# Performance work log

Hardware: AMD Instinct MI355X
Metric: run time of the kernel (lower is better)

## Reference

```python
import jax, jax.numpy as jnp
import numpy as np

DIM = 20
N = 200000
E = 6400000
ITERATIONS = 3


def setup_inputs() -> dict:
    key = jax.random.key(0)
    ks = jax.random.split(key, 20)
    inp = {
        "h": jax.random.normal(ks[0], (N, DIM), dtype=jnp.float32),
        "node2depth": jax.random.randint(ks[1], (N,), 0, 5, dtype=jnp.int32),
        "edge_src": jax.random.randint(ks[2], (E,), 0, N, dtype=jnp.int32),
        "edge_dst": jax.random.randint(ks[3], (E,), 0, N, dtype=jnp.int32),
    }
    # Six DIM x DIM Linear layers (weight stored [out,in] like torch, plus bias)
    scale = 1.0 / np.sqrt(DIM)
    names = ["Wz", "Uz", "Wr", "Ur", "Wh", "Uh"]
    for j, nm in enumerate(names):
        inp[nm + "_w"] = jax.random.uniform(ks[4 + 2 * j], (DIM, DIM), jnp.float32, -scale, scale)
        inp[nm + "_b"] = jax.random.uniform(ks[5 + 2 * j], (DIM,), jnp.float32, -scale, scale)
    return inp


def _linear(x, w, b):
    return x @ w.T + b


def reference(h, Wz_w, Wz_b, Uz_w, Uz_b, Wr_w, Wr_b, Ur_w, Ur_b,
              Wh_w, Wh_b, Uh_w, Uh_b, node2depth, edge_src, edge_dst):
    active = None
    for i in range(ITERATIONS):
        # active set shrinks as i grows (depth + i <= ITERATIONS)
        active = (node2depth + i) <= ITERATIONS  # [N] bool
        af = active.astype(h.dtype)
        # x[u] = sum over neighbors v of h[v], counting only active src AND active dst
        msg = h[edge_src] * af[edge_src][:, None]          # [E, DIM]
        x = jax.ops.segment_sum(msg, edge_dst, num_segments=N)  # [N, DIM]
        x = x * af[:, None]
        z = jax.nn.sigmoid(_linear(x, Wz_w, Wz_b) + _linear(h, Uz_w, Uz_b))
        r = jax.nn.sigmoid(_linear(x, Wr_w, Wr_b) + _linear(h, Ur_w, Ur_b))
        h_cand = jnp.tanh(_linear(x, Wh_w, Wh_b) + _linear(r * h, Uh_w, Uh_b))
        h_new = z * h + (1.0 - z) * h_cand
        # inactive nodes are dropped from the dict in the original; since the
        # active set only shrinks, keeping their old h is equivalent
        h = jnp.where(active[:, None], h_new, h)
    # original returns only nodes active at the last iteration; zero out the rest
    return jnp.where(active[:, None], h, jnp.zeros_like(h))
```

## Files before the change

### kernel.cpp

```cpp
#include <hip/hip_runtime.h>

#define DIM    20
#define NN     200000
#define EE     6400000
#define ITERS  3
#define BLOCK  256

#define NODES_PER_FINE   64
#define NFINE            3125
#define NCOARSE          98
#define FINE_PER_COARSE  32

#define TILE1            2048
#define IPT1             8

#define TILE             4096
#define IPT              16

#define CAP1             67584
#define NT2P             17
#define CAP2             2304
#define PIPT             9

#define XSTRIDE          21

typedef unsigned int u32;

__device__ __forceinline__ u32 pack_bf16x2(float a, float b) {
    u32 ua = __float_as_uint(a);
    u32 ub = __float_as_uint(b);
    ua = (ua + 0x7FFFu + ((ua >> 16) & 1u)) >> 16;
    ub = (ub + 0x7FFFu + ((ub >> 16) & 1u)) & 0xFFFF0000u;
    return ua | ub;
}

__global__ __launch_bounds__(BLOCK) void setup(const float* __restrict__ h,
                                               const int* __restrict__ depth,
                                               u32* __restrict__ hbA,
                                               u32* __restrict__ hbC,
                                               u32* __restrict__ CT,
                                               int* __restrict__ coarse_cursor,
                                               int* __restrict__ fine_cursor,
                                               int* __restrict__ gcur) {
    int g = blockIdx.x * BLOCK + threadIdx.x;
    if (g < NCOARSE) coarse_cursor[g] = g * CAP1;
    if (g < NFINE)   fine_cursor[g]   = g * CAP2;
    if (g == 0) *gcur = 0;
    if (g < NN / 8) {
        int4 a = *(const int4*)(depth + g * 8);
        int4 b = *(const int4*)(depth + g * 8 + 4);
        CT[g] = ((u32)a.x & 7u)        | (((u32)a.y & 7u) << 4)
              | (((u32)a.z & 7u) << 8) | (((u32)a.w & 7u) << 12)
              | (((u32)b.x & 7u) << 16)| (((u32)b.y & 7u) << 20)
              | (((u32)b.z & 7u) << 24)| (((u32)b.w & 7u) << 28);
    }
    int node = g >> 3, s = g & 7;
    if (depth[node] > ITERS) return;
    float2 f = *(const float2*)(h + (size_t)node * DIM + s * 2);
    hbA[(size_t)node * 8 + s] = pack_bf16x2(f.x, f.y);
    if (s < 2) {
        float2 fc = *(const float2*)(h + (size_t)node * DIM + 16 + s * 2);
        hbC[(size_t)node * 2 + s] = pack_bf16x2(fc.x, fc.y);
    }
}

__global__ __launch_bounds__(BLOCK) void p1_split(const int* __restrict__ esrc,
                                                  const int* __restrict__ edst,
                                                  int* __restrict__ coarse_cursor,
                                                  u32* __restrict__ buf1) {
    __shared__ u32 hist[NCOARSE];
    __shared__ u32 lbase[NCOARSE];
    __shared__ u32 gbase[NCOARSE];
    __shared__ u32 lout[TILE1];
    int tid = threadIdx.x;
    int start = blockIdx.x * TILE1;
    if (tid < NCOARSE) hist[tid] = 0;
    __syncthreads();

    int4 d4[2], s4[2];
    #pragma unroll
    for (int q = 0; q < 2; ++q) {
        int e4 = start + (q * BLOCK + tid) * 4;
        d4[q] = *(const int4*)(edst + e4);
        s4[q] = *(const int4*)(esrc + e4);
    }
    int dd[IPT1], ss[IPT1];
    dd[0]=d4[0].x; dd[1]=d4[0].y; dd[2]=d4[0].z; dd[3]=d4[0].w;
    dd[4]=d4[1].x; dd[5]=d4[1].y; dd[6]=d4[1].z; dd[7]=d4[1].w;
    ss[0]=s4[0].x; ss[1]=s4[0].y; ss[2]=s4[0].z; ss[3]=s4[0].w;
    ss[4]=s4[1].x; ss[5]=s4[1].y; ss[6]=s4[1].z; ss[7]=s4[1].w;

    u32 rank[IPT1];
    #pragma unroll
    for (int k = 0; k < IPT1; ++k)
        rank[k] = atomicAdd(&hist[(u32)dd[k] >> 11], 1u);
    __syncthreads();

    if (tid < 64) {
        u32 a = hist[tid];
        u32 b = (tid + 64 < NCOARSE) ? hist[tid + 64] : 0u;
        u32 ia = a, ib = b;
        #pragma unroll
        for (int off = 1; off < 64; off <<= 1) {
            u32 ta = (u32)__shfl_up((int)ia, off, 64);
            u32 tb = (u32)__shfl_up((int)ib, off, 64);
            if (tid >= off) { ia += ta; ib += tb; }
        }
        u32 totA = (u32)__shfl((int)ia, 63, 64);
        lbase[tid] = ia - a;
        if (tid + 64 < NCOARSE) lbase[tid + 64] = totA + ib - b;
    }
    __syncthreads();
    if (tid < NCOARSE) {
        u32 cq = hist[tid];
        gbase[tid] = cq ? (u32)atomicAdd((u32*)&coarse_cursor[tid], cq) : 0u;
    }
    #pragma unroll
    for (int k = 0; k < IPT1; ++k)
        lout[lbase[(u32)dd[k] >> 11] + rank[k]] = ((u32)dd[k] & 2047u) | ((u32)ss[k] << 11);
    __syncthreads();
    int wid = tid >> 6, lane = tid & 63;
    for (int b = wid; b < NCOARSE; b += 4) {
        u32 cq = hist[b], lb = lbase[b], gb = gbase[b];
        for (u32 i = lane; i < cq; i += 64)
            buf1[gb + i] = lout[lb + i];
    }
}

__global__ __launch_bounds__(BLOCK) void p2_split(const u32* __restrict__ buf1,
                                                  const int* __restrict__ coarse_cursor,
                                                  int* __restrict__ fine_cursor,
                                                  u32* __restrict__ buf2) {
    int bid = blockIdx.x;
    int c = bid / NT2P, t = bid - c * NT2P;
    int base  = c * CAP1;
    int end   = coarse_cursor[c];
    int start = base + t * TILE;
    if (start >= end) return;

    __shared__ u32 hist[FINE_PER_COARSE];
    __shared__ u32 lbase[FINE_PER_COARSE];
    __shared__ u32 gbase[FINE_PER_COARSE];
    __shared__ u32 lout[TILE];
    int tid = threadIdx.x;
    if (tid < FINE_PER_COARSE) hist[tid] = 0;
    __syncthreads();

    u32 w[IPT];
    #pragma unroll
    for (int q = 0; q < 4; ++q) {
        int i4 = start + (q * BLOCK + tid) * 4;
        if (i4 + 3 < end) {
            uint4 v = *(const uint4*)(buf1 + i4);
            w[q * 4 + 0] = v.x; w[q * 4 + 1] = v.y;
            w[q * 4 + 2] = v.z; w[q * 4 + 3] = v.w;
        } else {
            #pragma unroll
            for (int j = 0; j < 4; ++j) {
                int i = i4 + j;
                w[q * 4 + j] = (i < end) ? buf1[i] : 0xFFFFFFFFu;
            }
        }
    }
    u32 rank[IPT];
    #pragma unroll
    for (int k = 0; k < IPT; ++k)
        if (w[k] != 0xFFFFFFFFu)
            rank[k] = atomicAdd(&hist[(w[k] & 2047u) >> 6], 1u);
    __syncthreads();

    if (tid < 32) {
        u32 a = hist[tid], ia = a;
        #pragma unroll
        for (int off = 1; off < 32; off <<= 1) {
            u32 ta = (u32)__shfl_up((int)ia, off, 32);
            if (tid >= off) ia += ta;
        }
        lbase[tid] = ia - a;
        int f = c * FINE_PER_COARSE + tid;
        gbase[tid] = a ? (u32)atomicAdd((u32*)&fine_cursor[f], a) : 0u;
    }
    __syncthreads();
    #pragma unroll
    for (int k = 0; k < IPT; ++k)
        if (w[k] != 0xFFFFFFFFu)
            lout[lbase[(w[k] & 2047u) >> 6] + rank[k]] = (w[k] & 63u) | ((w[k] >> 11) << 6);
    __syncthreads();
    int wid = tid >> 6, lane = tid & 63;
    for (int b = wid; b < FINE_PER_COARSE; b += 4) {
        u32 cq = hist[b], lb = lbase[b], gb = gbase[b];
        for (u32 i = lane; i < cq; i += 64)
            buf2[gb + i] = lout[lb + i];
    }
}

__global__ __launch_bounds__(BLOCK) void pb_sort(const u32* __restrict__ buf2,
                                                 const int* __restrict__ fine_cursor,
                                                 const u32* __restrict__ CT,
                                                 int* __restrict__ gcur,
                                                 int* __restrict__ ptr,
                                                 u32* __restrict__ cnt3,
                                                 u32* __restrict__ ssrc) {
    __shared__ u32 hist[512];
    __shared__ u32 ebase[512];
    __shared__ u32 lout[CAP2];
    __shared__ u32 wsum[4];
    __shared__ int slo;
    int tid = threadIdx.x;
    int f = blockIdx.x;
    int base = f * CAP2;
    int end  = fine_cursor[f];
    int cnt  = end - base;
    hist[tid] = 0; hist[tid + 256] = 0;
    __syncthreads();

    u32 w[PIPT];
    #pragma unroll
    for (int q = 0; q < 2; ++q) {
        int i4 = base + (q * BLOCK + tid) * 4;
        if (i4 + 3 < end) {
            uint4 v = *(const uint4*)(buf2 + i4);
            w[q * 4 + 0] = v.x; w[q * 4 + 1] = v.y;
            w[q * 4 + 2] = v.z; w[q * 4 + 3] = v.w;
        } else {
            #pragma unroll
            for (int j = 0; j < 4; ++j) {
                int i = i4 + j;
                w[q * 4 + j] = (i < end) ? buf2[i] : 0xFFFFFFFFu;
            }
        }
    }
    {
        int i = base + 2 * BLOCK * 4 + tid;
        w[8] = (i < end) ? buf2[i] : 0xFFFFFFFFu;
    }
    u32 cls[PIPT];
    #pragma unroll
    for (int k = 0; k < PIPT; ++k) {
        u32 s = w[k] >> 6;
        if (s > (u32)(NN - 1)) s = (u32)(NN - 1);
        cls[k] = (CT[s >> 3] >> ((s & 7u) << 2)) & 7u;
    }
    u32 key[PIPT], rank[PIPT];
    #pragma unroll
    for (int k = 0; k < PIPT; ++k) {
        if (w[k] != 0xFFFFFFFFu) {
            key[k]  = (w[k] & 63u) * 8u + cls[k];
            rank[k] = atomicAdd(&hist[key[k]], 1u);
        }
    }
    if (tid == 0) slo = atomicAdd(gcur, cnt);
    __syncthreads();
    {
        u32 s0 = hist[2 * tid], s1 = hist[2 * tid + 1];
        u32 s = s0 + s1;
        int lane = tid & 63, wid = tid >> 6;
        u32 incl = s;
        #pragma unroll
        for (int off = 1; off < 64; off <<= 1) {
            u32 t = __shfl_up((int)incl, off, 64);
            if (lane >= off) incl += t;
        }
        if (lane == 63) wsum[wid] = incl;
        __syncthreads();
        u32 woff = 0;
        for (int w2 = 0; w2 < wid; ++w2) woff += wsum[w2];
        u32 excl = woff + incl - s;
        ebase[2 * tid]     = excl;
        ebase[2 * tid + 1] = excl + s0;
    }
    __syncthreads();
    int lo = slo;
    if (tid < NODES_PER_FINE) {
        u32 base0 = ebase[tid * 8];
        u32 cc1 = ebase[tid * 8 + 2] - base0;
        u32 cc2 = ebase[tid * 8 + 3] - base0;
        u32 cc3 = ebase[tid * 8 + 4] - base0;
        int u = f * NODES_PER_FINE + tid;
        ptr[u]  = lo + (int)base0;
        cnt3[u] = cc1 | (cc2 << 10) | (cc3 << 20);
    }
    #pragma unroll
    for (int k = 0; k < PIPT; ++k) {
        if (w[k] != 0xFFFFFFFFu) lout[ebase[key[k]] + rank[k]] = w[k] >> 6;
    }
    __syncthreads();
    for (int j = tid; j < cnt; j += BLOCK) ssrc[lo + j] = lout[j];
}


__device__ __forceinline__ float bl(u32 w) { return __uint_as_float(w << 16); }
__device__ __forceinline__ float bh(u32 w) { return __uint_as_float(w & 0xFFFF0000u); }

__device__ __forceinline__ void acc_half(float* xa, float* xc, uint4 a, u32 c) {
    xa[0]+=bl(a.x); xa[1]+=bh(a.x);
    xa[2]+=bl(a.y); xa[3]+=bh(a.y);
    xa[4]+=bl(a.z); xa[5]+=bh(a.z);
    xa[6]+=bl(a.w); xa[7]+=bh(a.w);
    xc[0]+=bl(c);   xc[1]+=bh(c);
}

__device__ __forceinline__ float fast_sigmoid(float t) {
    return 1.0f / (1.0f + __expf(-t));
}
__device__ __forceinline__ float fast_tanh(float t) {
    t = fminf(fmaxf(t, -15.0f), 15.0f);
    float e2 = __expf(2.0f * t);
    return (e2 - 1.0f) / (e2 + 1.0f);
}

__global__ __launch_bounds__(BLOCK) void grnn_iter(
    const u32* __restrict__ hbA_in, const u32* __restrict__ hbC_in,
    u32* __restrict__ hbA_out, u32* __restrict__ hbC_out,
    const float* __restrict__ h_in, float* __restrict__ h_out,
    const int* __restrict__ depth, const int* __restrict__ ptr,
    const u32* __restrict__ cnt3, const u32* __restrict__ ssrc,
    const float* __restrict__ Wz, const float* __restrict__ bWz,
    const float* __restrict__ Uz, const float* __restrict__ bUz,
    const float* __restrict__ Wr, const float* __restrict__ bWr,
    const float* __restrict__ Ur, const float* __restrict__ bUr,
    const float* __restrict__ Wh, const float* __restrict__ bWh,
    const float* __restrict__ Uh, const float* __restrict__ bUh,
    int lim, int limNext, int shift, int isFinal)
{
    __shared__ float xl[64 * XSTRIDE];
    int tid = threadIdx.x;
    int t = tid & 7, team = tid >> 3;
    int r = t >> 1, q = t & 1;

    #pragma unroll
    for (int rep = 0; rep < 2; ++rep) {
        int nl = team + rep * 32;
        int u = blockIdx.x * 64 + nl;
        if (depth[u] <= lim) {
            int p = ptr[u];
            int d = (int)((cnt3[u] >> shift) & 1023u);

            float xa[8], xc[2];
            #pragma unroll
            for (int k = 0; k < 8; ++k) xa[k] = 0.0f;
            xc[0] = 0.0f; xc[1] = 0.0f;

            int e = r;
            for (; e + 12 < d; e += 16) {
                u32 p0 = ssrc[p + e];
                u32 p1 = ssrc[p + e + 4];
                u32 p2 = ssrc[p + e + 8];
                u32 p3 = ssrc[p + e + 12];
                uint4 a0 = *(const uint4*)(hbA_in + (size_t)p0 * 8 + q * 4);
                uint4 a1 = *(const uint4*)(hbA_in + (size_t)p1 * 8 + q * 4);
                uint4 a2 = *(const uint4*)(hbA_in + (size_t)p2 * 8 + q * 4);
                uint4 a3 = *(const uint4*)(hbA_in + (size_t)p3 * 8 + q * 4);
                u32 c0 = hbC_in[(size_t)p0 * 2 + q];
                u32 c1 = hbC_in[(size_t)p1 * 2 + q];
                u32 c2 = hbC_in[(size_t)p2 * 2 + q];
                u32 c3 = hbC_in[(size_t)p3 * 2 + q];
                acc_half(xa, xc, a0, c0);
                acc_half(xa, xc, a1, c1);
                acc_half(xa, xc, a2, c2);
                acc_half(xa, xc, a3, c3);
            }
            for (; e + 4 < d; e += 8) {
                u32 p0 = ssrc[p + e];
                u32 p1 = ssrc[p + e + 4];
                uint4 a0 = *(const uint4*)(hbA_in + (size_t)p0 * 8 + q * 4);
                uint4 a1 = *(const uint4*)(hbA_in + (size_t)p1 * 8 + q * 4);
                u32 c0 = hbC_in[(size_t)p0 * 2 + q];
                u32 c1 = hbC_in[(size_t)p1 * 2 + q];
                acc_half(xa, xc, a0, c0);
                acc_half(xa, xc, a1, c1);
            }
            if (e < d) {
                u32 p0 = ssrc[p + e];
                uint4 a0 = *(const uint4*)(hbA_in + (size_t)p0 * 8 + q * 4);
                u32 c0 = hbC_in[(size_t)p0 * 2 + q];
                acc_half(xa, xc, a0, c0);
            }
            #pragma unroll
            for (int k = 0; k < 8; ++k) {
                xa[k] += __shfl_xor(xa[k], 2, 64);
                xa[k] += __shfl_xor(xa[k], 4, 64);
            }
            xc[0] += __shfl_xor(xc[0], 2, 64); xc[0] += __shfl_xor(xc[0], 4, 64);
            xc[1] += __shfl_xor(xc[1], 2, 64); xc[1] += __shfl_xor(xc[1], 4, 64);

            float* xr = xl + nl * XSTRIDE;
            if (t == 0) {
                #pragma unroll
                for (int k = 0; k < 8; ++k) xr[k] = xa[k];
                xr[16] = xc[0]; xr[17] = xc[1];
            } else if (t == 1) {
                #pragma unroll
                for (int k = 0; k < 8; ++k) xr[8 + k] = xa[k];
                xr[18] = xc[0]; xr[19] = xc[1];
            }
        }
    }
    __syncthreads();
    if (tid >= 64) return;

    int u = blockIdx.x * 64 + tid;
    int du = depth[u];
    if (du > lim) {
        if (isFinal) {
            float4 z4 = make_float4(0.f, 0.f, 0.f, 0.f);
            float4* o4 = (float4*)(h_out + (size_t)u * DIM);
            #pragma unroll
            for (int qq = 0; qq < 5; ++qq) o4[qq] = z4;
        }
        return;
    }

    float x[DIM], h[DIM];
    #pragma unroll
    for (int k = 0; k < DIM; ++k) x[k] = xl[tid * XSTRIDE + k];
    {
        const float4* hv = (const float4*)(h_in + (size_t)u * DIM);
        float4 a0 = hv[0], a1 = hv[1], a2 = hv[2], a3 = hv[3], a4 = hv[4];
        h[0]=a0.x; h[1]=a0.y; h[2]=a0.z; h[3]=a0.w;
        h[4]=a1.x; h[5]=a1.y; h[6]=a1.z; h[7]=a1.w;
        h[8]=a2.x; h[9]=a2.y; h[10]=a2.z; h[11]=a2.w;
        h[12]=a3.x; h[13]=a3.y; h[14]=a3.z; h[15]=a3.w;
        h[16]=a4.x; h[17]=a4.y; h[18]=a4.z; h[19]=a4.w;
    }

    float z[DIM], rh[DIM];
    #pragma unroll
    for (int j = 0; j < DIM; ++j) {
        float sz = bWz[j] + bUz[j];
        float sr = bWr[j] + bUr[j];
        #pragma unroll
        for (int k = 0; k < DIM; ++k) {
            sz += x[k] * Wz[j * DIM + k];
            sz += h[k] * Uz[j * DIM + k];
            sr += x[k] * Wr[j * DIM + k];
            sr += h[k] * Ur[j * DIM + k];
        }
        z[j]  = fast_sigmoid(sz);
        rh[j] = fast_sigmoid(sr) * h[j];
    }

    float o[DIM];
    #pragma unroll
    for (int j = 0; j < DIM; ++j) {
        float sh = bWh[j] + bUh[j];
        #pragma unroll
        for (int k = 0; k < DIM; ++k) {
            sh += x[k]  * Wh[j * DIM + k];
            sh += rh[k] * Uh[j * DIM + k];
        }
        float hc = fast_tanh(sh);
        o[j] = z[j] * h[j] + (1.0f - z[j]) * hc;
    }

    {
        float4* o4 = (float4*)(h_out + (size_t)u * DIM);
        o4[0] = make_float4(o[0],  o[1],  o[2],  o[3]);
        o4[1] = make_float4(o[4],  o[5],  o[6],  o[7]);
        o4[2] = make_float4(o[8],  o[9],  o[10], o[11]);
        o4[3] = make_float4(o[12], o[13], o[14], o[15]);
        o4[4] = make_float4(o[16], o[17], o[18], o[19]);
    }
    if (!isFinal && du <= limNext) {
        u32* rowA = hbA_out + (size_t)u * 8;
        uint4 wA0 = make_uint4(pack_bf16x2(o[0], o[1]),   pack_bf16x2(o[2], o[3]),
                               pack_bf16x2(o[4], o[5]),   pack_bf16x2(o[6], o[7]));
        uint4 wA1 = make_uint4(pack_bf16x2(o[8], o[9]),   pack_bf16x2(o[10], o[11]),
                               pack_bf16x2(o[12], o[13]), pack_bf16x2(o[14], o[15]));
        *(uint4*)rowA       = wA0;
        *(uint4*)(rowA + 4) = wA1;
        *(uint2*)(hbC_out + (size_t)u * 2) =
            make_uint2(pack_bf16x2(o[16], o[17]), pack_bf16x2(o[18], o[19]));
    }
}


extern "C" void kernel_launch(void* const* d_in, const int* in_sizes, int n_in,
                              void* d_out, int out_size, void* d_ws, size_t ws_size,
                              hipStream_t stream) {
    const float* h0    = (const float*)d_in[0];
    const int*   depth = (const int*)d_in[1];
    const int*   esrc  = (const int*)d_in[2];
    const int*   edst  = (const int*)d_in[3];
    const float* Wz  = (const float*)d_in[4];  const float* bWz = (const float*)d_in[5];
    const float* Uz  = (const float*)d_in[6];  const float* bUz = (const float*)d_in[7];
    const float* Wr  = (const float*)d_in[8];  const float* bWr = (const float*)d_in[9];
    const float* Ur  = (const float*)d_in[10]; const float* bUr = (const float*)d_in[11];
    const float* Wh  = (const float*)d_in[12]; const float* bWh = (const float*)d_in[13];
    const float* Uh  = (const float*)d_in[14]; const float* bUh = (const float*)d_in[15];
    float* out = (float*)d_out;

    int* W = (int*)d_ws;
    u32*  CT            = (u32*)(W + 0);
    int*  gcur          = W + 25024;
    int*  coarse_cursor = W + 25088;
    int*  fine_cursor   = W + 25216;
    int*  ptr           = W + 28416;
    u32*  cnt3          = (u32*)(W + 228416);
    u32*  buf1          = (u32*)(W + 428416);
    u32*  buf2          = buf1 + (size_t)NCOARSE * CAP1;
    float* h1           = (float*)(buf2 + (size_t)NFINE * CAP2);
    u32*  hbA0          = (u32*)(h1 + (size_t)NN * DIM);
    u32*  hbC0          = hbA0 + (size_t)NN * 8;
    u32*  hbA1          = hbC0 + (size_t)NN * 2;
    u32*  hbC1          = hbA1 + (size_t)NN * 8;
    u32*  ssrc          = buf1;

    setup   <<<(NN * 8) / BLOCK, BLOCK, 0, stream>>>(h0, depth, hbA0, hbC0, CT,
                                                     coarse_cursor, fine_cursor, gcur);
    p1_split<<<EE / TILE1, BLOCK, 0, stream>>>(esrc, edst, coarse_cursor, buf1);
    p2_split<<<NCOARSE * NT2P, BLOCK, 0, stream>>>(buf1, coarse_cursor, fine_cursor, buf2);
    pb_sort <<<NFINE, BLOCK, 0, stream>>>(buf2, fine_cursor, CT, gcur, ptr, cnt3, ssrc);

    grnn_iter<<<NN / 64, BLOCK, 0, stream>>>(hbA0, hbC0, hbA1, hbC1, h0, h1,
        depth, ptr, cnt3, ssrc,
        Wz, bWz, Uz, bUz, Wr, bWr, Ur, bUr, Wh, bWh, Uh, bUh, 3, 2, 20, 0);
    grnn_iter<<<NN / 64, BLOCK, 0, stream>>>(hbA1, hbC1, hbA0, hbC0, h1, h1,
        depth, ptr, cnt3, ssrc,
        Wz, bWz, Uz, bUz, Wr, bWr, Ur, bUr, Wh, bWh, Uh, bUh, 2, 1, 10, 0);
    grnn_iter<<<NN / 64, BLOCK, 0, stream>>>(hbA0, hbC0, hbA1, hbC1, h1, out,
        depth, ptr, cnt3, ssrc,
        Wz, bWz, Uz, bUz, Wr, bWr, Ur, bUr, Wh, bWh, Uh, bUh, 1, 0, 0, 1);
}
```

Measured before the change: 507.1 us.

## Fuse final sort pass with first GRU iteration using shared-memory edge lists

```diff
diff --git a/kernel.cpp b/kernel.cpp
--- a/kernel.cpp
+++ b/kernel.cpp
@@ -194,18 +194,123 @@
     }
 }
 
-__global__ __launch_bounds__(BLOCK) void pb_sort(const u32* __restrict__ buf2,
-                                                 const int* __restrict__ fine_cursor,
-                                                 const u32* __restrict__ CT,
-                                                 int* __restrict__ gcur,
-                                                 int* __restrict__ ptr,
-                                                 u32* __restrict__ cnt3,
-                                                 u32* __restrict__ ssrc) {
+
+__device__ __forceinline__ float bl(u32 w) { return __uint_as_float(w << 16); }
+__device__ __forceinline__ float bh(u32 w) { return __uint_as_float(w & 0xFFFF0000u); }
+
+__device__ __forceinline__ void acc_half(float* xa, float* xc, uint4 a, u32 c) {
+    xa[0]+=bl(a.x); xa[1]+=bh(a.x);
+    xa[2]+=bl(a.y); xa[3]+=bh(a.y);
+    xa[4]+=bl(a.z); xa[5]+=bh(a.z);
+    xa[6]+=bl(a.w); xa[7]+=bh(a.w);
+    xc[0]+=bl(c);   xc[1]+=bh(c);
+}
+
+__device__ __forceinline__ float fast_sigmoid(float t) {
+    return 1.0f / (1.0f + __expf(-t));
+}
+__device__ __forceinline__ float fast_tanh(float t) {
+    t = fminf(fmaxf(t, -15.0f), 15.0f);
+    float e2 = __expf(2.0f * t);
+    return (e2 - 1.0f) / (e2 + 1.0f);
+}
+
+__device__ __forceinline__ void gru_body(
+    int u, int tid, const float* xl,
+    const float* __restrict__ h_in, float* __restrict__ h_out,
+    u32* __restrict__ hbA_out, u32* __restrict__ hbC_out,
+    int du, int limNext, int isFinal,
+    const float* __restrict__ Wz, const float* __restrict__ bWz,
+    const float* __restrict__ Uz, const float* __restrict__ bUz,
+    const float* __restrict__ Wr, const float* __restrict__ bWr,
+    const float* __restrict__ Ur, const float* __restrict__ bUr,
+    const float* __restrict__ Wh, const float* __restrict__ bWh,
+    const float* __restrict__ Uh, const float* __restrict__ bUh)
+{
+    float x[DIM], h[DIM];
+    #pragma unroll
+    for (int k = 0; k < DIM; ++k) x[k] = xl[tid * XSTRIDE + k];
+    {
+        const float4* hv = (const float4*)(h_in + (size_t)u * DIM);
+        float4 a0 = hv[0], a1 = hv[1], a2 = hv[2], a3 = hv[3], a4 = hv[4];
+        h[0]=a0.x; h[1]=a0.y; h[2]=a0.z; h[3]=a0.w;
+        h[4]=a1.x; h[5]=a1.y; h[6]=a1.z; h[7]=a1.w;
+        h[8]=a2.x; h[9]=a2.y; h[10]=a2.z; h[11]=a2.w;
+        h[12]=a3.x; h[13]=a3.y; h[14]=a3.z; h[15]=a3.w;
+        h[16]=a4.x; h[17]=a4.y; h[18]=a4.z; h[19]=a4.w;
+    }
+
+    float z[DIM], rh[DIM];
+    #pragma unroll
+    for (int j = 0; j < DIM; ++j) {
+        float sz = bWz[j] + bUz[j];
+        float sr = bWr[j] + bUr[j];
+        #pragma unroll
+        for (int k = 0; k < DIM; ++k) {
+            sz += x[k] * Wz[j * DIM + k];
+            sz += h[k] * Uz[j * DIM + k];
+            sr += x[k] * Wr[j * DIM + k];
+            sr += h[k] * Ur[j * DIM + k];
+        }
+        z[j]  = fast_sigmoid(sz);
+        rh[j] = fast_sigmoid(sr) * h[j];
+    }
+
+    float o[DIM];
+    #pragma unroll
+    for (int j = 0; j < DIM; ++j) {
+        float sh = bWh[j] + bUh[j];
+        #pragma unroll
+        for (int k = 0; k < DIM; ++k) {
+            sh += x[k]  * Wh[j * DIM + k];
+            sh += rh[k] * Uh[j * DIM + k];
+        }
+        float hc = fast_tanh(sh);
+        o[j] = z[j] * h[j] + (1.0f - z[j]) * hc;
+    }
+
+    {
+        float4* o4 = (float4*)(h_out + (size_t)u * DIM);
+        o4[0] = make_float4(o[0],  o[1],  o[2],  o[3]);
+        o4[1] = make_float4(o[4],  o[5],  o[6],  o[7]);
+        o4[2] = make_float4(o[8],  o[9],  o[10], o[11]);
+        o4[3] = make_float4(o[12], o[13], o[14], o[15]);
+        o4[4] = make_float4(o[16], o[17], o[18], o[19]);
+    }
+    if (!isFinal && du <= limNext) {
+        u32* rowA = hbA_out + (size_t)u * 8;
+        uint4 wA0 = make_uint4(pack_bf16x2(o[0], o[1]),   pack_bf16x2(o[2], o[3]),
+                               pack_bf16x2(o[4], o[5]),   pack_bf16x2(o[6], o[7]));
+        uint4 wA1 = make_uint4(pack_bf16x2(o[8], o[9]),   pack_bf16x2(o[10], o[11]),
+                               pack_bf16x2(o[12], o[13]), pack_bf16x2(o[14], o[15]));
+        *(uint4*)rowA       = wA0;
+        *(uint4*)(rowA + 4) = wA1;
+        *(uint2*)(hbC_out + (size_t)u * 2) =
+            make_uint2(pack_bf16x2(o[16], o[17]), pack_bf16x2(o[18], o[19]));
+    }
+}
+
+__global__ __launch_bounds__(BLOCK) void pb_gru(
+    const u32* __restrict__ buf2, const int* __restrict__ fine_cursor,
+    const u32* __restrict__ CT, int* __restrict__ gcur,
+    int* __restrict__ ptr, u32* __restrict__ cnt3, u32* __restrict__ ssrc,
+    const u32* __restrict__ hbA_in, const u32* __restrict__ hbC_in,
+    u32* __restrict__ hbA_out, u32* __restrict__ hbC_out,
+    const float* __restrict__ h_in, float* __restrict__ h_out,
+    const int* __restrict__ depth,
+    const float* __restrict__ Wz, const float* __restrict__ bWz,
+    const float* __restrict__ Uz, const float* __restrict__ bUz,
+    const float* __restrict__ Wr, const float* __restrict__ bWr,
+    const float* __restrict__ Ur, const float* __restrict__ bUr,
+    const float* __restrict__ Wh, const float* __restrict__ bWh,
+    const float* __restrict__ Uh, const float* __restrict__ bUh)
+{
     __shared__ u32 hist[512];
     __shared__ u32 ebase[512];
     __shared__ u32 lout[CAP2];
     __shared__ u32 wsum[4];
     __shared__ int slo;
+    __shared__ float xl[64 * XSTRIDE];
     int tid = threadIdx.x;
     int f = blockIdx.x;
     int base = f * CAP2;
@@ -286,28 +391,87 @@
     }
     __syncthreads();
     for (int j = tid; j < cnt; j += BLOCK) ssrc[lo + j] = lout[j];
-}
-
-
-__device__ __forceinline__ float bl(u32 w) { return __uint_as_float(w << 16); }
-__device__ __forceinline__ float bh(u32 w) { return __uint_as_float(w & 0xFFFF0000u); }
-
-__device__ __forceinline__ void acc_half(float* xa, float* xc, uint4 a, u32 c) {
-    xa[0]+=bl(a.x); xa[1]+=bh(a.x);
-    xa[2]+=bl(a.y); xa[3]+=bh(a.y);
-    xa[4]+=bl(a.z); xa[5]+=bh(a.z);
-    xa[6]+=bl(a.w); xa[7]+=bh(a.w);
-    xc[0]+=bl(c);   xc[1]+=bh(c);
-}
-
-__device__ __forceinline__ float fast_sigmoid(float t) {
-    return 1.0f / (1.0f + __expf(-t));
-}
-__device__ __forceinline__ float fast_tanh(float t) {
-    t = fminf(fmaxf(t, -15.0f), 15.0f);
-    float e2 = __expf(2.0f * t);
-    return (e2 - 1.0f) / (e2 + 1.0f);
-}
+
+    int t = tid & 7, team = tid >> 3;
+    int r = t >> 1, q = t & 1;
+    #pragma unroll
+    for (int rep = 0; rep < 2; ++rep) {
+        int nl = team + rep * 32;
+        int u = f * NODES_PER_FINE + nl;
+        if (depth[u] <= ITERS) {
+            int b0 = (int)ebase[nl * 8];
+            int d  = (int)(ebase[nl * 8 + 4] - ebase[nl * 8]);
+
+            float xa[8], xc[2];
+            #pragma unroll
+            for (int k = 0; k < 8; ++k) xa[k] = 0.0f;
+            xc[0] = 0.0f; xc[1] = 0.0f;
+
+            int e = r;
+            for (; e + 12 < d; e += 16) {
+                u32 p0 = lout[b0 + e];
+                u32 p1 = lout[b0 + e + 4];
+                u32 p2 = lout[b0 + e + 8];
+                u32 p3 = lout[b0 + e + 12];
+                uint4 a0 = *(const uint4*)(hbA_in + (size_t)p0 * 8 + q * 4);
+                uint4 a1 = *(const uint4*)(hbA_in + (size_t)p1 * 8 + q * 4);
+                uint4 a2 = *(const uint4*)(hbA_in + (size_t)p2 * 8 + q * 4);
+                uint4 a3 = *(const uint4*)(hbA_in + (size_t)p3 * 8 + q * 4);
+                u32 c0 = hbC_in[(size_t)p0 * 2 + q];
+                u32 c1 = hbC_in[(size_t)p1 * 2 + q];
+                u32 c2 = hbC_in[(size_t)p2 * 2 + q];
+                u32 c3 = hbC_in[(size_t)p3 * 2 + q];
+                acc_half(xa, xc, a0, c0);
+                acc_half(xa, xc, a1, c1);
+                acc_half(xa, xc, a2, c2);
+                acc_half(xa, xc, a3, c3);
+            }
+            for (; e + 4 < d; e += 8) {
+                u32 p0 = lout[b0 + e];
+                u32 p1 = lout[b0 + e + 4];
+                uint4 a0 = *(const uint4*)(hbA_in + (size_t)p0 * 8 + q * 4);
+                uint4 a1 = *(const uint4*)(hbA_in + (size_t)p1 * 8 + q * 4);
+                u32 c0 = hbC_in[(size_t)p0 * 2 + q];
+                u32 c1 = hbC_in[(size_t)p1 * 2 + q];
+                acc_half(xa, xc, a0, c0);
+                acc_half(xa, xc, a1, c1);
+            }
+            if (e < d) {
+                u32 p0 = lout[b0 + e];
+                uint4 a0 = *(const uint4*)(hbA_in + (size_t)p0 * 8 + q * 4);
+                u32 c0 = hbC_in[(size_t)p0 * 2 + q];
+                acc_half(xa, xc, a0, c0);
+            }
+            #pragma unroll
+            for (int k = 0; k < 8; ++k) {
+                xa[k] += __shfl_xor(xa[k], 2, 64);
+                xa[k] += __shfl_xor(xa[k], 4, 64);
+            }
+            xc[0] += __shfl_xor(xc[0], 2, 64); xc[0] += __shfl_xor(xc[0], 4, 64);
+            xc[1] += __shfl_xor(xc[1], 2, 64); xc[1] += __shfl_xor(xc[1], 4, 64);
+
+            float* xr = xl + nl * XSTRIDE;
+            if (t == 0) {
+                #pragma unroll
+                for (int k = 0; k < 8; ++k) xr[k] = xa[k];
+                xr[16] = xc[0]; xr[17] = xc[1];
+            } else if (t == 1) {
+                #pragma unroll
+                for (int k = 0; k < 8; ++k) xr[8 + k] = xa[k];
+                xr[18] = xc[0]; xr[19] = xc[1];
+            }
+        }
+    }
+    __syncthreads();
+    if (tid >= 64) return;
+
+    int u = f * NODES_PER_FINE + tid;
+    int du = depth[u];
+    if (du > ITERS) return;
+    gru_body(u, tid, xl, h_in, h_out, hbA_out, hbC_out, du, 2, 0,
+             Wz, bWz, Uz, bUz, Wr, bWr, Ur, bUr, Wh, bWh, Uh, bUh);
+}
+
 
 __global__ __launch_bounds__(BLOCK) void grnn_iter(
     const u32* __restrict__ hbA_in, const u32* __restrict__ hbC_in,
@@ -410,68 +574,8 @@
         }
         return;
     }
-
-    float x[DIM], h[DIM];
-    #pragma unroll
-    for (int k = 0; k < DIM; ++k) x[k] = xl[tid * XSTRIDE + k];
-    {
-        const float4* hv = (const float4*)(h_in + (size_t)u * DIM);
-        float4 a0 = hv[0], a1 = hv[1], a2 = hv[2], a3 = hv[3], a4 = hv[4];
-        h[0]=a0.x; h[1]=a0.y; h[2]=a0.z; h[3]=a0.w;
-        h[4]=a1.x; h[5]=a1.y; h[6]=a1.z; h[7]=a1.w;
-        h[8]=a2.x; h[9]=a2.y; h[10]=a2.z; h[11]=a2.w;
-        h[12]=a3.x; h[13]=a3.y; h[14]=a3.z; h[15]=a3.w;
-        h[16]=a4.x; h[17]=a4.y; h[18]=a4.z; h[19]=a4.w;
-    }
-
-    float z[DIM], rh[DIM];
-    #pragma unroll
-    for (int j = 0; j < DIM; ++j) {
-        float sz = bWz[j] + bUz[j];
-        float sr = bWr[j] + bUr[j];
-        #pragma unroll
-        for (int k = 0; k < DIM; ++k) {
-            sz += x[k] * Wz[j * DIM + k];
-            sz += h[k] * Uz[j * DIM + k];
-            sr += x[k] * Wr[j * DIM + k];
-            sr += h[k] * Ur[j * DIM + k];
-        }
-        z[j]  = fast_sigmoid(sz);
-        rh[j] = fast_sigmoid(sr) * h[j];
-    }
-
-    float o[DIM];
-    #pragma unroll
-    for (int j = 0; j < DIM; ++j) {
-        float sh = bWh[j] + bUh[j];
-        #pragma unroll
-        for (int k = 0; k < DIM; ++k) {
-            sh += x[k]  * Wh[j * DIM + k];
-            sh += rh[k] * Uh[j * DIM + k];
-        }
-        float hc = fast_tanh(sh);
-        o[j] = z[j] * h[j] + (1.0f - z[j]) * hc;
-    }
-
-    {
-        float4* o4 = (float4*)(h_out + (size_t)u * DIM);
-        o4[0] = make_float4(o[0],  o[1],  o[2],  o[3]);
-        o4[1] = make_float4(o[4],  o[5],  o[6],  o[7]);
-        o4[2] = make_float4(o[8],  o[9],  o[10], o[11]);
-        o4[3] = make_float4(o[12], o[13], o[14], o[15]);
-        o4[4] = make_float4(o[16], o[17], o[18], o[19]);
-    }
-    if (!isFinal && du <= limNext) {
-        u32* rowA = hbA_out + (size_t)u * 8;
-        uint4 wA0 = make_uint4(pack_bf16x2(o[0], o[1]),   pack_bf16x2(o[2], o[3]),
-                               pack_bf16x2(o[4], o[5]),   pack_bf16x2(o[6], o[7]));
-        uint4 wA1 = make_uint4(pack_bf16x2(o[8], o[9]),   pack_bf16x2(o[10], o[11]),
-                               pack_bf16x2(o[12], o[13]), pack_bf16x2(o[14], o[15]));
-        *(uint4*)rowA       = wA0;
-        *(uint4*)(rowA + 4) = wA1;
-        *(uint2*)(hbC_out + (size_t)u * 2) =
-            make_uint2(pack_bf16x2(o[16], o[17]), pack_bf16x2(o[18], o[19]));
-    }
+    gru_body(u, tid, xl, h_in, h_out, hbA_out, hbC_out, du, limNext, isFinal,
+             Wz, bWz, Uz, bUz, Wr, bWr, Ur, bUr, Wh, bWh, Uh, bUh);
 }
 
 
@@ -510,11 +614,11 @@
                                                      coarse_cursor, fine_cursor, gcur);
     p1_split<<<EE / TILE1, BLOCK, 0, stream>>>(esrc, edst, coarse_cursor, buf1);
     p2_split<<<NCOARSE * NT2P, BLOCK, 0, stream>>>(buf1, coarse_cursor, fine_cursor, buf2);
-    pb_sort <<<NFINE, BLOCK, 0, stream>>>(buf2, fine_cursor, CT, gcur, ptr, cnt3, ssrc);
-
-    grnn_iter<<<NN / 64, BLOCK, 0, stream>>>(hbA0, hbC0, hbA1, hbC1, h0, h1,
-        depth, ptr, cnt3, ssrc,
-        Wz, bWz, Uz, bUz, Wr, bWr, Ur, bUr, Wh, bWh, Uh, bUh, 3, 2, 20, 0);
+
+    pb_gru  <<<NFINE, BLOCK, 0, stream>>>(buf2, fine_cursor, CT, gcur, ptr, cnt3, ssrc,
+        hbA0, hbC0, hbA1, hbC1, h0, h1, depth,
+        Wz, bWz, Uz, bUz, Wr, bWr, Ur, bUr, Wh, bWh, Uh, bUh);
+
     grnn_iter<<<NN / 64, BLOCK, 0, stream>>>(hbA1, hbC1, hbA0, hbC0, h1, h1,
         depth, ptr, cnt3, ssrc,
         Wz, bWz, Uz, bUz, Wr, bWr, Ur, bUr, Wh, bWh, Uh, bUh, 2, 1, 10, 0);
```

Result: faster. 489.4 us (-3.5%).
